# Kernel tuning notes

Hardware: AMD Instinct MI355X
Metric: run time of the kernel (lower is better)

The kernel has to match this reference:

```python
import jax, jax.numpy as jnp
import numpy as np

B, T, C = 4, 4096, 128

def setup_inputs() -> dict:
    key = jax.random.key(0)
    k1, k2, k3, k4 = jax.random.split(key, 4)
    x = jax.random.normal(k1, (B, T, C), dtype=jnp.float32)
    s = 1.0 / np.sqrt(C)
    Wq = jax.random.normal(k2, (C, C), dtype=jnp.float32) * s
    Wk = jax.random.normal(k3, (C, C), dtype=jnp.float32) * s
    Wv = jax.random.normal(k4, (C, C), dtype=jnp.float32) * s
    return {"x": x, "Wq": Wq, "Wk": Wk, "Wv": Wv}

def reference(x, Wq, Wk, Wv):
    # nn.Linear(bias=False): y = x @ W.T
    q = jnp.einsum('btc,dc->btd', x, Wq)
    k = jnp.einsum('btc,dc->btd', x, Wk)
    v = jnp.einsum('btc,dc->btd', x, Wv)
    scale = 1.0 / jnp.sqrt(jnp.asarray(x.shape[-1], x.dtype))
    att = jnp.einsum('btd,bsd->bts', q, k) * scale  # [B,T,T]
    causal = jnp.tril(jnp.ones((x.shape[1], x.shape[1]), dtype=bool))
    att = jnp.where(causal[None, :, :], att, -jnp.inf)
    w = jax.nn.softmax(att, axis=-1)
    # dropout p=0.0 -> identity
    out = jnp.einsum('bts,bsd->btd', w, v)
    return out
```

## Files before the change

kernel.cpp:

```cpp
#include <hip/hip_runtime.h>
#include <hip/hip_bf16.h>
#include <math.h>

#define T_SEQ 4096
#define C_DIM 128
#define B_SZ  4

typedef __attribute__((ext_vector_type(8))) short short8;
typedef __attribute__((ext_vector_type(4))) short short4v;
typedef __attribute__((ext_vector_type(4))) float f32x4;

__device__ __forceinline__ short f2bf(float f) {
    union { float fv; unsigned u; } v; v.fv = f;
    unsigned r = v.u + 0x7fff + ((v.u >> 16) & 1);
    return (short)(r >> 16);
}

__device__ __forceinline__ unsigned pk_bf16(float a, float b) {
    union { __hip_bfloat162 h2; unsigned u; } c;
    c.h2 = __float22bfloat162_rn(make_float2(a, b));
    return c.u;
}

__device__ __forceinline__ short8 load_f32x8_bf16(const float* p) {
    const float4* q = (const float4*)p;
    float4 a = q[0], b = q[1];
    short8 r;
    r[0] = f2bf(a.x); r[1] = f2bf(a.y); r[2] = f2bf(a.z); r[3] = f2bf(a.w);
    r[4] = f2bf(b.x); r[5] = f2bf(b.y); r[6] = f2bf(b.z); r[7] = f2bf(b.w);
    return r;
}

__device__ __forceinline__ void async_cp16(const short* g, short* l) {
    __builtin_amdgcn_global_load_lds(
        (const __attribute__((address_space(1))) unsigned int*)g,
        (__attribute__((address_space(3))) unsigned int*)l, 16, 0, 0);
}

__global__ __launch_bounds__(512) void qkv_proj(
    const float* __restrict__ x, const float* __restrict__ Wq,
    const float* __restrict__ Wk, const float* __restrict__ Wv,
    short* __restrict__ Q, short* __restrict__ Kf, short* __restrict__ Vf)
{
    __shared__ short8 Wl[2048];

    const int tid  = threadIdx.x;
    const int lane = tid & 63;
    const int ln15 = lane & 15;
    const int quad = lane >> 4;
    const int mat  = blockIdx.x >> 6;
    const int rt   = (blockIdx.x & 63) * 8 + (tid >> 6);
    const int m0   = rt * 32;

    const float* W = (mat == 0) ? Wq : (mat == 1) ? Wk : Wv;

    for (int i = tid; i < 2048; i += 512) {
        int n = i >> 4, kc = i & 15;
        short8 v = load_f32x8_bf16(W + n * C_DIM + kc * 8);
        Wl[((n >> 4) * 4 + (kc >> 2)) * 64 + (kc & 3) * 16 + (n & 15)] = v;
    }

    short8 afr[2][4];
#pragma unroll
    for (int ms = 0; ms < 2; ++ms) {
        const float* xrow = x + (size_t)(m0 + ms * 16 + ln15) * C_DIM + quad * 8;
#pragma unroll
        for (int ks = 0; ks < 4; ++ks)
            afr[ms][ks] = load_f32x8_bf16(xrow + ks * 32);
    }

    __syncthreads();

    const float scale = (mat == 0) ? (0.08838834764831845f * 1.4426950408889634f)
                                   : 1.0f;
    const int b  = m0 >> 12;
    const int tl = m0 & 4095;

#pragma unroll
    for (int nt = 0; nt < 8; ++nt) {
        f32x4 acc0 = {0.f, 0.f, 0.f, 0.f};
        f32x4 acc1 = {0.f, 0.f, 0.f, 0.f};
#pragma unroll
        for (int ks = 0; ks < 4; ++ks) {
            short8 bfr = Wl[(nt * 4 + ks) * 64 + lane];
            if (mat == 2) {
                acc0 = __builtin_amdgcn_mfma_f32_16x16x32_bf16(afr[0][ks], bfr, acc0, 0, 0, 0);
                acc1 = __builtin_amdgcn_mfma_f32_16x16x32_bf16(afr[1][ks], bfr, acc1, 0, 0, 0);
            } else {
                acc0 = __builtin_amdgcn_mfma_f32_16x16x32_bf16(bfr, afr[0][ks], acc0, 0, 0, 0);
                acc1 = __builtin_amdgcn_mfma_f32_16x16x32_bf16(bfr, afr[1][ks], acc1, 0, 0, 0);
            }
        }
        if (mat == 0) {
            short4v s0, s1;
#pragma unroll
            for (int r = 0; r < 4; ++r) { s0[r] = f2bf(acc0[r] * scale); s1[r] = f2bf(acc1[r] * scale); }
            *(short4v*)&Q[(size_t)(m0 + ln15) * C_DIM + nt * 16 + quad * 4]      = s0;
            *(short4v*)&Q[(size_t)(m0 + 16 + ln15) * C_DIM + nt * 16 + quad * 4] = s1;
        } else if (mat == 1) {
            const int t16 = tl >> 4;
            short4v s0, s1;
#pragma unroll
            for (int r = 0; r < 4; ++r) { s0[r] = f2bf(acc0[r]); s1[r] = f2bf(acc1[r]); }
            size_t base = (((size_t)(b * 256 + t16) * 4 + (nt >> 1)) << 9)
                        + (((nt & 1) * 2 + (quad >> 1)) * 128) + ln15 * 8 + (quad & 1) * 4;
            *(short4v*)&Kf[base]        = s0;
            *(short4v*)&Kf[base + 2048] = s1;
        } else {
            const int kvc = tl >> 5;
            short4v s0, s1;
#pragma unroll
            for (int r = 0; r < 4; ++r) { s0[r] = f2bf(acc0[r]); s1[r] = f2bf(acc1[r]); }
            short* vbase = Vf + (((size_t)(b * 128 + kvc) * 8 + nt) << 9);
            *(short4v*)&vbase[((quad >> 1) * 16 + ln15) * 8 + (quad & 1) * 4]       = s0;
            *(short4v*)&vbase[(((quad >> 1) + 2) * 16 + ln15) * 8 + (quad & 1) * 4] = s1;
        }
    }
}


#define ROUND_BODY(KC, VC, KN, VN, R)                                        \
  {                                                                          \
    const int kv0 = (R) << 6;                                                \
     \
    asm volatile("s_waitcnt vmcnt(0)" ::: "memory");                         \
    __builtin_amdgcn_sched_barrier(0);                                       \
    __builtin_amdgcn_s_barrier();                                            \
    __builtin_amdgcn_sched_barrier(0);                                       \
    if ((R) + 2 <= kmax) {                                                   \
      const short* gk = Kb + ((size_t)((R) + 2) << 13) + w * 2048;           \
      const short* gv = Vb + ((size_t)((R) + 2) << 13) + w * 2048;           \
      _Pragma("unroll")                                                      \
      for (int i = 0; i < 4; ++i) {                                          \
        async_cp16(gk + i * 512 + lane * 8, &KN[w * 2048 + i * 512]);        \
        async_cp16(gv + i * 512 + lane * 8, &VN[w * 2048 + i * 512]);        \
      }                                                                      \
    }                                                                        \
             \
    short8 kfr[4];                                                           \
    _Pragma("unroll")                                                        \
    for (int ks = 0; ks < 4; ++ks)                                           \
      kfr[ks] = *(const short8*)&KC[(w * 4 + ks) * 512 + lane * 8];          \
    f32x4 St[2];                                                             \
    _Pragma("unroll")                                                        \
    for (int qt = 0; qt < 2; ++qt) {                                         \
      f32x4 s = {0.f, 0.f, 0.f, 0.f};                                        \
      _Pragma("unroll")                                                      \
      for (int ks = 0; ks < 4; ++ks)                                         \
        s = __builtin_amdgcn_mfma_f32_16x16x32_bf16(kfr[ks], qf[qt][ks], s,  \
                                                    0, 0, 0);                \
      St[qt] = s;                                                            \
    }                                                                        \
    if (kv0 + 64 > q0) {                                                     \
      _Pragma("unroll")                                                      \
      for (int qt = 0; qt < 2; ++qt) {                                       \
        int qcol = q0 + qt * 16 + ln15;                                      \
        _Pragma("unroll")                                                    \
        for (int rr = 0; rr < 4; ++rr)                                       \
          if (kv0 + w * 16 + quad * 4 + rr > qcol) St[qt][rr] = -INFINITY;   \
      }                                                                      \
    }                                                                        \
    _Pragma("unroll")                                                        \
    for (int qt = 0; qt < 2; ++qt) {                                         \
      float p0 = __builtin_amdgcn_exp2f(St[qt][0] - 16.f);                   \
      float p1 = __builtin_amdgcn_exp2f(St[qt][1] - 16.f);                   \
      float p2 = __builtin_amdgcn_exp2f(St[qt][2] - 16.f);                   \
      float p3 = __builtin_amdgcn_exp2f(St[qt][3] - 16.f);                   \
      l_i[qt] += (p0 + p1) + (p2 + p3);                                      \
      uint2 pk;                                                              \
      pk.x = pk_bf16(p0, p1);                                                \
      pk.y = pk_bf16(p2, p3);                                                \
      *(uint2*)&Plds[(qt * 16 + ln15) * 68 + w * 16 + quad * 4] = pk;        \
    }                                                                        \
            \
    asm volatile("s_waitcnt lgkmcnt(0)" ::: "memory");                       \
    __builtin_amdgcn_sched_barrier(0);                                       \
    __builtin_amdgcn_s_barrier();                                            \
    __builtin_amdgcn_sched_barrier(0);                                       \
          \
    _Pragma("unroll")                                                        \
    for (int kc = 0; kc < 2; ++kc) {                                         \
      short8 vfr[2];                                                         \
      _Pragma("unroll")                                                      \
      for (int di = 0; di < 2; ++di)                                         \
        vfr[di] =                                                            \
            *(const short8*)&VC[(kc * 8 + w * 2 + di) * 512 + lane * 8];     \
      _Pragma("unroll")                                                      \
      for (int qi = 0; qi < 2; ++qi) {                                       \
        short8 pf = *(const short8*)&Plds[(qi * 16 + ln15) * 68              \
                                          + kc * 32 + quad * 8];             \
        _Pragma("unroll")                                                    \
        for (int di = 0; di < 2; ++di)                                       \
          acc[qi][di] = __builtin_amdgcn_mfma_f32_16x16x32_bf16(             \
              vfr[di], pf, acc[qi][di], 0, 0, 0);                            \
      }                                                                      \
    }                                                                        \
  }

__global__ __launch_bounds__(256, 2) void flash_attn(
    const short* __restrict__ Q, const short* __restrict__ Kf,
    const short* __restrict__ Vf, float* __restrict__ part,
    float* __restrict__ lpart)
{
    __shared__ short Klds0[8192];
    __shared__ short Klds1[8192];
    __shared__ short Vlds0[8192];
    __shared__ short Vlds1[8192];
    __shared__ short Plds[32 * 68];
    __shared__ float lsum[32];

    const int tid  = threadIdx.x;
    const int w    = tid >> 6;
    const int lane = tid & 63;
    const int ln15 = lane & 15;
    const int quad = lane >> 4;
    const int bid  = blockIdx.x;
    const int x    = bid & 7;
    const int b    = x >> 1;
    const int h    = x & 1;
    const int j    = bid >> 3;

    const short* Qb = Q  + (size_t)b * T_SEQ * C_DIM;
    const short* Kb = Kf + ((size_t)b << 19);
    const short* Vb = Vf + ((size_t)b << 19);

    for (int half = 0; half < 2; ++half) {
        const int qc   = half ? (127 - j) : j;
        const int q0   = qc * 32;
        const int kmax = (q0 + 31) >> 6;

        short8 qf[2][4];
#pragma unroll
        for (int qt = 0; qt < 2; ++qt) {
            const short* qrow = Qb + (size_t)(q0 + qt * 16 + ln15) * C_DIM + quad * 8;
#pragma unroll
            for (int ks = 0; ks < 4; ++ks)
                qf[qt][ks] = *(const short8*)(qrow + ks * 32);
        }

        f32x4 acc[2][2];
#pragma unroll
        for (int qi = 0; qi < 2; ++qi)
#pragma unroll
            for (int di = 0; di < 2; ++di)
                acc[qi][di] = (f32x4){0.f, 0.f, 0.f, 0.f};
        float l_i[2] = {0.f, 0.f};

        if (h <= kmax) {
            const short* gk = Kb + ((size_t)h << 13) + w * 2048;
            const short* gv = Vb + ((size_t)h << 13) + w * 2048;
#pragma unroll
            for (int i = 0; i < 4; ++i) {
                async_cp16(gk + i * 512 + lane * 8, &Klds0[w * 2048 + i * 512]);
                async_cp16(gv + i * 512 + lane * 8, &Vlds0[w * 2048 + i * 512]);
            }
        }

        int r = h;
        while (r <= kmax) {
            ROUND_BODY(Klds0, Vlds0, Klds1, Vlds1, r);
            r += 2;
            if (r > kmax) break;
            ROUND_BODY(Klds1, Vlds1, Klds0, Vlds0, r);
            r += 2;
        }

        __syncthreads();
        if (tid < 32) lsum[tid] = 0.f;
        __syncthreads();
#pragma unroll
        for (int qt = 0; qt < 2; ++qt)
            atomicAdd(&lsum[qt * 16 + ln15], l_i[qt]);
        __syncthreads();

        const size_t pb = (size_t)(h * 4 + b) * 524288 + (size_t)q0 * 128;
#pragma unroll
        for (int qi = 0; qi < 2; ++qi)
#pragma unroll
            for (int di = 0; di < 2; ++di) {
                float4 v = make_float4(acc[qi][di][0], acc[qi][di][1],
                                       acc[qi][di][2], acc[qi][di][3]);
                *(float4*)&part[pb + (qi * 16 + ln15) * 128
                                + (w * 2 + di) * 16 + quad * 4] = v;
            }
        if (tid < 32)
            lpart[(size_t)(h * 4 + b) * 4096 + q0 + tid] = lsum[tid];
        __syncthreads();
    }
}

__global__ __launch_bounds__(256) void combine(
    const float* __restrict__ part, const float* __restrict__ lpart,
    float* __restrict__ out)
{
    const int tid = threadIdx.x;
    const int bid = blockIdx.x;
    const size_t PLANE  = (size_t)4 * 64 * 8192;
    const size_t LPLANE = (size_t)4 * 64 * 64;

#pragma unroll
    for (int i = 0; i < 8; ++i) {
        int f4  = bid * 2048 + i * 256 + tid;
        int c4  = f4 & 31;
        int row = f4 >> 5;
        int b   = row >> 12;
        int t   = row & 4095;
        int qc  = t >> 6;
        int qr  = t & 63;
        size_t base = (size_t)((b * 64 + qc)) * 8192 + qr * 128 + c4 * 4;
        float4 p0 = *(const float4*)&part[base];
        float4 p1 = *(const float4*)&part[base + PLANE];
        float  l  = lpart[(size_t)(b * 64 + qc) * 64 + qr]
                  + lpart[(size_t)(b * 64 + qc) * 64 + qr + LPLANE];
        float li = 1.0f / l;
        float4 v;
        v.x = (p0.x + p1.x) * li;
        v.y = (p0.y + p1.y) * li;
        v.z = (p0.z + p1.z) * li;
        v.w = (p0.w + p1.w) * li;
        ((float4*)out)[f4] = v;
    }
}

extern "C" void kernel_launch(void* const* d_in, const int* in_sizes, int n_in,
                              void* d_out, int out_size, void* d_ws, size_t ws_size,
                              hipStream_t stream) {
    const float* x  = (const float*)d_in[0];
    const float* Wq = (const float*)d_in[1];
    const float* Wk = (const float*)d_in[2];
    const float* Wv = (const float*)d_in[3];
    float* out = (float*)d_out;

    const size_t elems = (size_t)B_SZ * T_SEQ * C_DIM;
    short* Q  = (short*)d_ws;
    short* Kf = Q  + elems;
    short* Vf = Kf + elems;
    float* part  = (float*)(Vf + elems);
    float* lpart = part + (size_t)2 * 4 * 64 * 8192;

    hipLaunchKernelGGL(qkv_proj, dim3(192), dim3(512), 0, stream,
                       x, Wq, Wk, Wv, Q, Kf, Vf);
    hipLaunchKernelGGL(flash_attn, dim3(512), dim3(256), 0, stream,
                       Q, Kf, Vf, part, lpart);
    hipLaunchKernelGGL(combine, dim3(256), dim3(256), 0, stream,
                       part, lpart, out);
}
```

Measured before the change: 121.5 us.

## Drop split-KV partials and combine kernel; use 8-wave blocks over all KV tiles

The old version split each query chunk's KV range across two blocks, wrote fp32 partial outputs and row sums to workspace, and merged them in a separate combine kernel. Now each block of 512 threads (two groups of four waves, one group per 16 query rows) walks every KV tile itself and writes the normalized output directly. This removes the partial-buffer traffic and one kernel launch. In exchange there are half as many blocks, each with a longer serial KV loop, so parallelism is lower and load balance across CUs may suffer.

```diff
diff --git a/kernel.cpp b/kernel.cpp
--- a/kernel.cpp
+++ b/kernel.cpp
@@ -127,198 +127,142 @@
     __builtin_amdgcn_sched_barrier(0);                                       \
     __builtin_amdgcn_s_barrier();                                            \
     __builtin_amdgcn_sched_barrier(0);                                       \
-    if ((R) + 2 <= kmax) {                                                   \
-      const short* gk = Kb + ((size_t)((R) + 2) << 13) + w * 2048;           \
-      const short* gv = Vb + ((size_t)((R) + 2) << 13) + w * 2048;           \
-      _Pragma("unroll")                                                      \
-      for (int i = 0; i < 4; ++i) {                                          \
-        async_cp16(gk + i * 512 + lane * 8, &KN[w * 2048 + i * 512]);        \
-        async_cp16(gv + i * 512 + lane * 8, &VN[w * 2048 + i * 512]);        \
+    if ((R) + 1 <= kmax) {                                                   \
+      const short* gk = Kb + ((size_t)((R) + 1) << 13) + w * 1024;           \
+      const short* gv = Vb + ((size_t)((R) + 1) << 13) + w * 1024;           \
+      _Pragma("unroll")                                                      \
+      for (int i = 0; i < 2; ++i) {                                          \
+        async_cp16(gk + i * 512 + lane * 8, &KN[w * 1024 + i * 512]);        \
+        async_cp16(gv + i * 512 + lane * 8, &VN[w * 1024 + i * 512]);        \
       }                                                                      \
     }                                                                        \
-             \
+     \
     short8 kfr[4];                                                           \
     _Pragma("unroll")                                                        \
     for (int ks = 0; ks < 4; ++ks)                                           \
-      kfr[ks] = *(const short8*)&KC[(w * 4 + ks) * 512 + lane * 8];          \
-    f32x4 St[2];                                                             \
+      kfr[ks] = *(const short8*)&KC[(wg * 4 + ks) * 512 + lane * 8];         \
+    f32x4 St = {0.f, 0.f, 0.f, 0.f};                                         \
     _Pragma("unroll")                                                        \
-    for (int qt = 0; qt < 2; ++qt) {                                         \
-      f32x4 s = {0.f, 0.f, 0.f, 0.f};                                        \
-      _Pragma("unroll")                                                      \
-      for (int ks = 0; ks < 4; ++ks)                                         \
-        s = __builtin_amdgcn_mfma_f32_16x16x32_bf16(kfr[ks], qf[qt][ks], s,  \
-                                                    0, 0, 0);                \
-      St[qt] = s;                                                            \
-    }                                                                        \
+    for (int ks = 0; ks < 4; ++ks)                                           \
+      St = __builtin_amdgcn_mfma_f32_16x16x32_bf16(kfr[ks], qf[ks], St,      \
+                                                   0, 0, 0);                 \
     if (kv0 + 64 > q0) {                                                     \
-      _Pragma("unroll")                                                      \
-      for (int qt = 0; qt < 2; ++qt) {                                       \
-        int qcol = q0 + qt * 16 + ln15;                                      \
-        _Pragma("unroll")                                                    \
-        for (int rr = 0; rr < 4; ++rr)                                       \
-          if (kv0 + w * 16 + quad * 4 + rr > qcol) St[qt][rr] = -INFINITY;   \
-      }                                                                      \
-    }                                                                        \
-    _Pragma("unroll")                                                        \
-    for (int qt = 0; qt < 2; ++qt) {                                         \
-      float p0 = __builtin_amdgcn_exp2f(St[qt][0] - 16.f);                   \
-      float p1 = __builtin_amdgcn_exp2f(St[qt][1] - 16.f);                   \
-      float p2 = __builtin_amdgcn_exp2f(St[qt][2] - 16.f);                   \
-      float p3 = __builtin_amdgcn_exp2f(St[qt][3] - 16.f);                   \
-      l_i[qt] += (p0 + p1) + (p2 + p3);                                      \
+      const int qcol = q0 + ln15;                                            \
+      _Pragma("unroll")                                                      \
+      for (int rr = 0; rr < 4; ++rr)                                         \
+        if (kv0 + wg * 16 + quad * 4 + rr > qcol) St[rr] = -INFINITY;        \
+    }                                                                        \
+    {                                                                        \
+      float p0 = __builtin_amdgcn_exp2f(St[0] - 16.f);                       \
+      float p1 = __builtin_amdgcn_exp2f(St[1] - 16.f);                       \
+      float p2 = __builtin_amdgcn_exp2f(St[2] - 16.f);                       \
+      float p3 = __builtin_amdgcn_exp2f(St[3] - 16.f);                       \
+      l_i += (p0 + p1) + (p2 + p3);                                          \
       uint2 pk;                                                              \
       pk.x = pk_bf16(p0, p1);                                                \
       pk.y = pk_bf16(p2, p3);                                                \
-      *(uint2*)&Plds[(qt * 16 + ln15) * 68 + w * 16 + quad * 4] = pk;        \
-    }                                                                        \
-            \
+      *(uint2*)&Plds[g][ln15 * 68 + wg * 16 + quad * 4] = pk;                \
+    }                                                                        \
+           \
     asm volatile("s_waitcnt lgkmcnt(0)" ::: "memory");                       \
     __builtin_amdgcn_sched_barrier(0);                                       \
     __builtin_amdgcn_s_barrier();                                            \
     __builtin_amdgcn_sched_barrier(0);                                       \
-          \
+           \
     _Pragma("unroll")                                                        \
     for (int kc = 0; kc < 2; ++kc) {                                         \
       short8 vfr[2];                                                         \
       _Pragma("unroll")                                                      \
       for (int di = 0; di < 2; ++di)                                         \
         vfr[di] =                                                            \
-            *(const short8*)&VC[(kc * 8 + w * 2 + di) * 512 + lane * 8];     \
-      _Pragma("unroll")                                                      \
-      for (int qi = 0; qi < 2; ++qi) {                                       \
-        short8 pf = *(const short8*)&Plds[(qi * 16 + ln15) * 68              \
-                                          + kc * 32 + quad * 8];             \
-        _Pragma("unroll")                                                    \
-        for (int di = 0; di < 2; ++di)                                       \
-          acc[qi][di] = __builtin_amdgcn_mfma_f32_16x16x32_bf16(             \
-              vfr[di], pf, acc[qi][di], 0, 0, 0);                            \
-      }                                                                      \
+            *(const short8*)&VC[(kc * 8 + wg * 2 + di) * 512 + lane * 8];    \
+      short8 pf = *(const short8*)&Plds[g][ln15 * 68 + kc * 32 + quad * 8];  \
+      _Pragma("unroll")                                                      \
+      for (int di = 0; di < 2; ++di)                                         \
+        acc[di] = __builtin_amdgcn_mfma_f32_16x16x32_bf16(                   \
+            vfr[di], pf, acc[di], 0, 0, 0);                                  \
     }                                                                        \
   }
 
-__global__ __launch_bounds__(256, 2) void flash_attn(
+__global__ __launch_bounds__(512, 2) void flash_attn(
     const short* __restrict__ Q, const short* __restrict__ Kf,
-    const short* __restrict__ Vf, float* __restrict__ part,
-    float* __restrict__ lpart)
+    const short* __restrict__ Vf, float* __restrict__ out)
 {
     __shared__ short Klds0[8192];
     __shared__ short Klds1[8192];
     __shared__ short Vlds0[8192];
     __shared__ short Vlds1[8192];
-    __shared__ short Plds[32 * 68];
-    __shared__ float lsum[32];
+    __shared__ short Plds[2][1088];
+    __shared__ float lsum[2][16];
 
     const int tid  = threadIdx.x;
     const int w    = tid >> 6;
     const int lane = tid & 63;
     const int ln15 = lane & 15;
     const int quad = lane >> 4;
+    const int g    = w >> 2;
+    const int wg   = w & 3;
     const int bid  = blockIdx.x;
-    const int x    = bid & 7;
-    const int b    = x >> 1;
-    const int h    = x & 1;
-    const int j    = bid >> 3;
+    const int b    = bid & 3;
+    const int jj   = bid >> 2;
 
     const short* Qb = Q  + (size_t)b * T_SEQ * C_DIM;
     const short* Kb = Kf + ((size_t)b << 19);
     const short* Vb = Vf + ((size_t)b << 19);
+    float* outb = out + (size_t)b * T_SEQ * C_DIM;
 
     for (int half = 0; half < 2; ++half) {
-        const int qc   = half ? (127 - j) : j;
-        const int q0   = qc * 32;
-        const int kmax = (q0 + 31) >> 6;
-
-        short8 qf[2][4];
-#pragma unroll
-        for (int qt = 0; qt < 2; ++qt) {
-            const short* qrow = Qb + (size_t)(q0 + qt * 16 + ln15) * C_DIM + quad * 8;
+        const int p    = half ? (127 - jj) : jj;
+        const int q0   = p * 32 + g * 16;
+        const int kmax = (p * 32 + 31) >> 6;
+
+        short8 qf[4];
+        {
+            const short* qrow = Qb + (size_t)(q0 + ln15) * C_DIM + quad * 8;
 #pragma unroll
             for (int ks = 0; ks < 4; ++ks)
-                qf[qt][ks] = *(const short8*)(qrow + ks * 32);
-        }
-
-        f32x4 acc[2][2];
-#pragma unroll
-        for (int qi = 0; qi < 2; ++qi)
-#pragma unroll
-            for (int di = 0; di < 2; ++di)
-                acc[qi][di] = (f32x4){0.f, 0.f, 0.f, 0.f};
-        float l_i[2] = {0.f, 0.f};
-
-        if (h <= kmax) {
-            const short* gk = Kb + ((size_t)h << 13) + w * 2048;
-            const short* gv = Vb + ((size_t)h << 13) + w * 2048;
-#pragma unroll
-            for (int i = 0; i < 4; ++i) {
-                async_cp16(gk + i * 512 + lane * 8, &Klds0[w * 2048 + i * 512]);
-                async_cp16(gv + i * 512 + lane * 8, &Vlds0[w * 2048 + i * 512]);
+                qf[ks] = *(const short8*)(qrow + ks * 32);
+        }
+
+        f32x4 acc[2];
+#pragma unroll
+        for (int di = 0; di < 2; ++di)
+            acc[di] = (f32x4){0.f, 0.f, 0.f, 0.f};
+        float l_i = 0.f;
+
+        {
+            const short* gk = Kb + w * 1024;
+            const short* gv = Vb + w * 1024;
+#pragma unroll
+            for (int i = 0; i < 2; ++i) {
+                async_cp16(gk + i * 512 + lane * 8, &Klds0[w * 1024 + i * 512]);
+                async_cp16(gv + i * 512 + lane * 8, &Vlds0[w * 1024 + i * 512]);
             }
         }
 
-        int r = h;
-        while (r <= kmax) {
+        int r = 0;
+        while (true) {
             ROUND_BODY(Klds0, Vlds0, Klds1, Vlds1, r);
-            r += 2;
-            if (r > kmax) break;
+            if (++r > kmax) break;
             ROUND_BODY(Klds1, Vlds1, Klds0, Vlds0, r);
-            r += 2;
-        }
-
-        __syncthreads();
-        if (tid < 32) lsum[tid] = 0.f;
-        __syncthreads();
-#pragma unroll
-        for (int qt = 0; qt < 2; ++qt)
-            atomicAdd(&lsum[qt * 16 + ln15], l_i[qt]);
-        __syncthreads();
-
-        const size_t pb = (size_t)(h * 4 + b) * 524288 + (size_t)q0 * 128;
-#pragma unroll
-        for (int qi = 0; qi < 2; ++qi)
-#pragma unroll
-            for (int di = 0; di < 2; ++di) {
-                float4 v = make_float4(acc[qi][di][0], acc[qi][di][1],
-                                       acc[qi][di][2], acc[qi][di][3]);
-                *(float4*)&part[pb + (qi * 16 + ln15) * 128
-                                + (w * 2 + di) * 16 + quad * 4] = v;
-            }
-        if (tid < 32)
-            lpart[(size_t)(h * 4 + b) * 4096 + q0 + tid] = lsum[tid];
-        __syncthreads();
-    }
-}
-
-__global__ __launch_bounds__(256) void combine(
-    const float* __restrict__ part, const float* __restrict__ lpart,
-    float* __restrict__ out)
-{
-    const int tid = threadIdx.x;
-    const int bid = blockIdx.x;
-    const size_t PLANE  = (size_t)4 * 64 * 8192;
-    const size_t LPLANE = (size_t)4 * 64 * 64;
-
-#pragma unroll
-    for (int i = 0; i < 8; ++i) {
-        int f4  = bid * 2048 + i * 256 + tid;
-        int c4  = f4 & 31;
-        int row = f4 >> 5;
-        int b   = row >> 12;
-        int t   = row & 4095;
-        int qc  = t >> 6;
-        int qr  = t & 63;
-        size_t base = (size_t)((b * 64 + qc)) * 8192 + qr * 128 + c4 * 4;
-        float4 p0 = *(const float4*)&part[base];
-        float4 p1 = *(const float4*)&part[base + PLANE];
-        float  l  = lpart[(size_t)(b * 64 + qc) * 64 + qr]
-                  + lpart[(size_t)(b * 64 + qc) * 64 + qr + LPLANE];
-        float li = 1.0f / l;
-        float4 v;
-        v.x = (p0.x + p1.x) * li;
-        v.y = (p0.y + p1.y) * li;
-        v.z = (p0.z + p1.z) * li;
-        v.w = (p0.w + p1.w) * li;
-        ((float4*)out)[f4] = v;
+            if (++r > kmax) break;
+        }
+
+        __syncthreads();
+        if (tid < 32) ((float*)lsum)[tid] = 0.f;
+        __syncthreads();
+        atomicAdd(&lsum[g][ln15], l_i);
+        __syncthreads();
+
+        const float li = 1.0f / lsum[g][ln15];
+        float* orow = outb + (size_t)(q0 + ln15) * C_DIM;
+#pragma unroll
+        for (int di = 0; di < 2; ++di) {
+            float4 v = make_float4(acc[di][0] * li, acc[di][1] * li,
+                                   acc[di][2] * li, acc[di][3] * li);
+            *(float4*)&orow[(wg * 2 + di) * 16 + quad * 4] = v;
+        }
+        __syncthreads();
     }
 }
 
@@ -335,13 +279,9 @@
     short* Q  = (short*)d_ws;
     short* Kf = Q  + elems;
     short* Vf = Kf + elems;
-    float* part  = (float*)(Vf + elems);
-    float* lpart = part + (size_t)2 * 4 * 64 * 8192;
 
     hipLaunchKernelGGL(qkv_proj, dim3(192), dim3(512), 0, stream,
                        x, Wq, Wk, Wv, Q, Kf, Vf);
-    hipLaunchKernelGGL(flash_attn, dim3(512), dim3(256), 0, stream,
-                       Q, Kf, Vf, part, lpart);
-    hipLaunchKernelGGL(combine, dim3(256), dim3(256), 0, stream,
-                       part, lpart, out);
-}
+    hipLaunchKernelGGL(flash_attn, dim3(256), dim3(512), 0, stream,
+                       Q, Kf, Vf, out);
+}
```

Result: slower. 131.4 us (+8.2%).
